# Performance work log

Measured on AMD Instinct MI355X. Metric: run time of the kernel, lower is better.

## Reference

```python
import jax, jax.numpy as jnp
import numpy as np

NUM_T = 1000      # diffusion timesteps
TIME_DIM = 16     # gaussian time embedding size
DIST_DIM = 16     # gaussian distance embedding size


def _gsmear(x, stop, num_g):
    # GaussianSmearing with linearly spaced centers in [0, stop]
    offsets = jnp.linspace(0.0, stop, num_g)
    coeff = -0.5 / (offsets[1] - offsets[0]) ** 2
    return jnp.exp(coeff * (x[:, None] - offsets[None, :]) ** 2)


def setup_inputs():
    key = jax.random.key(0)
    ks = jax.random.split(key, 20)
    N, EH, G = 20000, 100000, 1000          # nodes, halfedges, graphs
    NT, ND, ED, L, NE = 16, 256, 128, 2, 5   # node types, node_dim, edge_dim, blocks, edge types
    h_node = jax.nn.one_hot(jax.random.randint(ks[0], (N,), 0, NT), NT, dtype=jnp.float32)
    pos_node = jax.random.normal(ks[1], (N, 3), dtype=jnp.float32) * 3.0
    batch_node = jnp.sort(jax.random.randint(ks[2], (N,), 0, G))
    half = jax.random.randint(ks[3], (2, EH), 0, N)
    edge_index = jnp.concatenate([half, half[::-1]], axis=1)  # halfedges + flipped
    bh = jnp.sort(jax.random.randint(ks[4], (EH,), 0, G))
    batch_edge = jnp.concatenate([bh, bh], axis=0)
    t = jax.random.randint(ks[5], (G,), 0, NUM_T)

    def w(k, shape):
        fan_in = shape[-2] if len(shape) > 1 else shape[-1]
        return jax.random.normal(k, shape, dtype=jnp.float32) / np.sqrt(fan_in)

    e_in = ED + 2 * ND + DIST_DIM + 1
    return {
        'h_node': h_node, 'pos_node': pos_node, 'batch_node': batch_node,
        'edge_index': edge_index, 'batch_edge': batch_edge, 't': t,
        'W_node_emb': w(ks[6], (NT, ND - TIME_DIM)),
        'W_edge_emb': w(ks[7], (2 * NT, ED - TIME_DIM)),
        'We1': w(ks[8], (L, e_in, ED)), 'be1': jnp.zeros((L, ED), jnp.float32),
        'We2': w(ks[9], (L, ED, ED)), 'be2': jnp.zeros((L, ED), jnp.float32),
        'Wm': w(ks[10], (L, ND + ED, ND)), 'bm': jnp.zeros((L, ND), jnp.float32),
        'Wn1': w(ks[11], (L, 2 * ND + 1, ND)), 'bn1': jnp.zeros((L, ND), jnp.float32),
        'Wn2': w(ks[12], (L, ND, ND)), 'bn2': jnp.zeros((L, ND), jnp.float32),
        'Wd1': w(ks[13], (ED + ND, ED)), 'bd1': jnp.zeros((ED,), jnp.float32),
        'Wd2': w(ks[14], (ED, ED)), 'bd2': jnp.zeros((ED,), jnp.float32),
        'Wd3': w(ks[15], (ED, NE)), 'bd3': jnp.zeros((NE,), jnp.float32),
    }


def reference(h_node, pos_node, batch_node, edge_index, batch_edge, t,
              W_node_emb, W_edge_emb, We1, be1, We2, be2, Wm, bm,
              Wn1, bn1, Wn2, bn2, Wd1, bd1, Wd2, bd2, Wd3, bd3):
    src, dst = edge_index[0], edge_index[1]
    N = h_node.shape[0]
    L = We1.shape[0]

    # edge input features: concat of endpoint node features (gather)
    h_e0 = jnp.concatenate([h_node[src], h_node[dst]], axis=-1)

    tn = t[batch_node].astype(jnp.float32)  # per-node timestep
    te = t[batch_edge].astype(jnp.float32)  # per-edge timestep
    # linear embed + gaussian-smeared time embedding
    h_n = jnp.concatenate([h_node @ W_node_emb, _gsmear(tn, float(NUM_T), TIME_DIM)], axis=-1)
    h_e = jnp.concatenate([h_e0 @ W_edge_emb, _gsmear(te, float(NUM_T), TIME_DIM)], axis=-1)
    node_time = (tn / NUM_T)[:, None]
    edge_time = (te / NUM_T)[:, None]

    # geometric edge features
    d = jnp.linalg.norm(pos_node[dst] - pos_node[src], axis=-1)
    dist_emb = _gsmear(d, 10.0, DIST_DIM)

    # NodeEdgeNet: alternating edge / node residual updates
    for l in range(L):
        e_in = jnp.concatenate([h_e, h_n[src], h_n[dst], dist_emb, edge_time], axis=-1)
        h_e = h_e + jax.nn.relu(e_in @ We1[l] + be1[l]) @ We2[l] + be2[l]
        msg = jax.nn.relu(jnp.concatenate([h_n[src], h_e], axis=-1) @ Wm[l] + bm[l])
        agg = jax.ops.segment_sum(msg, dst, num_segments=N)
        n_in = jnp.concatenate([h_n, agg, node_time], axis=-1)
        h_n = h_n + jax.nn.relu(n_in @ Wn1[l] + bn1[l]) @ Wn2[l] + bn2[l]

    # symmetrize halfedges and decode edge types
    nh = h_e.shape[0] // 2
    h_ext = jnp.concatenate([h_e[:nh] + h_e[nh:],
                             h_n[src[:nh]] + h_n[dst[:nh]]], axis=-1)
    h = jax.nn.relu(h_ext @ Wd1 + bd1)
    h = jax.nn.relu(h @ Wd2 + bd2)
    return h @ Wd3 + bd3
```

## Files before the change

kernel.cpp:

```cpp
#include <hip/hip_runtime.h>
#include <math.h>


typedef __attribute__((ext_vector_type(8)))  short bf16x8;
typedef __attribute__((ext_vector_type(16))) float f32x16;

__device__ __forceinline__ float b2f(unsigned short u) {
    union { float f; unsigned int i; } x; x.i = ((unsigned int)u) << 16; return x.f;
}
__device__ __forceinline__ unsigned short f2b(float f) {
    union { float f; unsigned int i; } x; x.f = f;
    unsigned int r = x.i + 0x7fffu + ((x.i >> 16) & 1u);
    return (unsigned short)(r >> 16);
}
__device__ __forceinline__ bf16x8 ld8(const unsigned short* p) { return *(const bf16x8*)p; }
__device__ __forceinline__ bf16x8 zero8() { bf16x8 r = {0,0,0,0,0,0,0,0}; return r; }
__device__ __forceinline__ bf16x8 add8(bf16x8 a, bf16x8 b) {
    bf16x8 r;
#pragma unroll
    for (int j = 0; j < 8; j++) r[j] = (short)f2b(b2f((unsigned short)a[j]) + b2f((unsigned short)b[j]));
    return r;
}

#define MFMA4(ACC, A0, A1, B0, B1)                                                   \
    ACC[0][0] = __builtin_amdgcn_mfma_f32_32x32x16_bf16(A0, B0, ACC[0][0], 0, 0, 0); \
    ACC[0][1] = __builtin_amdgcn_mfma_f32_32x32x16_bf16(A0, B1, ACC[0][1], 0, 0, 0); \
    ACC[1][0] = __builtin_amdgcn_mfma_f32_32x32x16_bf16(A1, B0, ACC[1][0], 0, 0, 0); \
    ACC[1][1] = __builtin_amdgcn_mfma_f32_32x32x16_bf16(A1, B1, ACC[1][1], 0, 0, 0);

#define LANE_SETUP()                                  \
    const int tid  = threadIdx.x;                     \
    const int lane = tid & 63;                        \
    const int wave = tid >> 6;                        \
    const int wm = wave >> 1, wn = wave & 1;          \
    const int l31 = lane & 31, l5 = lane >> 5;        \
    (void)wm; (void)wn; (void)lane;

#define PIPELINE4(NITER, FETCH, ACC)                                  \
    {                                                                 \
        bf16x8 pa0[2], pb0[2], pa1[2], pb1[2], pa2[2], pb2[2];        \
        FETCH(0, pa0, pb0);                                           \
        if (1 < (NITER)) FETCH(1, pa1, pb1);                          \
        _Pragma("unroll")                                             \
        for (int i = 0; i < (NITER); i++) {                           \
            if (i + 2 < (NITER)) FETCH(i + 2, pa2, pb2);              \
            MFMA4(ACC, pa0[0], pa0[1], pb0[0], pb0[1]);               \
            pa0[0] = pa1[0]; pa0[1] = pa1[1];                         \
            pb0[0] = pb1[0]; pb0[1] = pb1[1];                         \
            pa1[0] = pa2[0]; pa1[1] = pa2[1];                         \
            pb1[0] = pb2[0]; pb1[1] = pb2[1];                         \
        }                                                             \
    }

__global__ void zero_i32_k(int* p, int n) {
    int i = blockIdx.x * 256 + threadIdx.x;
    if (i < n) p[i] = 0;
}
__global__ void hist_k(const int* __restrict__ dst, int* __restrict__ cnt, int E) {
    int e = blockIdx.x * 256 + threadIdx.x;
    if (e < E) atomicAdd(&cnt[dst[e]], 1);
}
__global__ __launch_bounds__(256) void scan_k(int* __restrict__ cnt, int N) {
    __shared__ int s[256];
    const int tidx  = threadIdx.x;
    const int chunk = (N + 255) / 256;
    const int lo = tidx * chunk;
    const int hi = (lo + chunk < N) ? lo + chunk : N;
    int sum = 0;
    for (int i = lo; i < hi; i++) sum += cnt[i];
    s[tidx] = sum;
    __syncthreads();
    for (int d = 1; d < 256; d <<= 1) {
        int t = (tidx >= d) ? s[tidx - d] : 0;
        __syncthreads();
        s[tidx] += t;
        __syncthreads();
    }
    int base = s[tidx] - sum;
    for (int i = lo; i < hi; i++) {
        int c = cnt[i];
        cnt[i] = base;
        base += c;
    }
}
__global__ void fill_k(const int* __restrict__ src, const int* __restrict__ dst,
                       const int* __restrict__ batch_edge, int* __restrict__ cur,
                       int* __restrict__ eids, int* __restrict__ pos,
                       int* __restrict__ srcp, int* __restrict__ dstp,
                       int* __restrict__ bep, int E) {
    int e = blockIdx.x * 256 + threadIdx.x;
    if (e < E) {
        int p = atomicAdd(&cur[dst[e]], 1);
        eids[p] = e;
        pos[e]  = p;
        srcp[p] = src[e];
        dstp[p] = dst[e];
        bep[p]  = batch_edge[e];
    }
}
__global__ void pad_k(int* eids, int* srcp, int* dstp, int* bep, int E, int Epad) {
    int i = E + blockIdx.x * 256 + threadIdx.x;
    if (i < Epad) { eids[i] = -1; srcp[i] = 0; dstp[i] = -1; bep[i] = 0; }
}

__global__ void typ_k(const float* __restrict__ h_node, int* __restrict__ typ, int N) {
    int i = blockIdx.x * 256 + threadIdx.x;
    if (i >= N) return;
    int ty = 0;
#pragma unroll
    for (int k = 0; k < 16; k++) if (h_node[i * 16 + k] > 0.5f) ty = k;
    typ[i] = ty;
}

struct TrDesc { const float* W; unsigned short* Wt; int K, N, Kpad; };
struct TrAll  { TrDesc d[12]; };

__global__ __launch_bounds__(256) void tr_all_k(TrAll a) {
    TrDesc t = a.d[blockIdx.y];
    int total = t.N * t.Kpad;
    for (int i = blockIdx.x * 256 + threadIdx.x; i < total; i += gridDim.x * 256) {
        int n = i / t.Kpad, k = i - n * t.Kpad;
        float v = (k < t.K) ? t.W[(size_t)k * t.N + n] : 0.f;
        t.Wt[(size_t)n * t.Kpad + k] = f2b(v);
    }
}

__global__ void embed_node_k(const int* __restrict__ typ,
                             const float* __restrict__ Wn,
                             const int* __restrict__ batch_node,
                             const int* __restrict__ t,
                             unsigned short* __restrict__ h_n, int N) {
    int idx = blockIdx.x * 256 + threadIdx.x;
    if (idx >= N * 32) return;
    int row = idx >> 5, seg = idx & 31;
    bf16x8 v;
    if (seg < 30) {
        const float* w = Wn + (size_t)typ[row] * 240 + seg * 8;
#pragma unroll
        for (int j = 0; j < 8; j++) v[j] = (short)f2b(w[j]);
    } else {
        float x = (float)t[batch_node[row]];
#pragma unroll
        for (int j = 0; j < 8; j++) {
            int col = seg * 8 + j;
            float dx = x - (1000.0f / 15.0f) * (float)(col - 240);
            v[j] = (short)f2b(expf(-1.125e-4f * dx * dx));
        }
    }
    *(bf16x8*)&h_n[(size_t)row * 256 + seg * 8] = v;
}

__global__ void embed_edge_k(const int* __restrict__ typ,
                             const float* __restrict__ We,
                             const int* __restrict__ srcp,
                             const int* __restrict__ dstp,
                             const int* __restrict__ bep,
                             const int* __restrict__ t,
                             unsigned short* __restrict__ h_e, int E) {
    int idx = blockIdx.x * 256 + threadIdx.x;
    if (idx >= E * 16) return;
    int row = idx >> 4, seg = idx & 15;
    bf16x8 v;
    if (seg < 14) {
        int d0 = dstp[row]; if (d0 < 0) d0 = 0;
        const float* ws = We + (size_t)typ[srcp[row]] * 112 + seg * 8;
        const float* wd = We + (size_t)(16 + typ[d0]) * 112 + seg * 8;
#pragma unroll
        for (int j = 0; j < 8; j++) v[j] = (short)f2b(ws[j] + wd[j]);
    } else {
        float x = (float)t[bep[row]];
#pragma unroll
        for (int j = 0; j < 8; j++) {
            int col = seg * 8 + j;
            float dx = x - (1000.0f / 15.0f) * (float)(col - 112);
            v[j] = (short)f2b(expf(-1.125e-4f * dx * dx));
        }
    }
    *(bf16x8*)&h_e[(size_t)row * 128 + seg * 8] = v;
}

__global__ __launch_bounds__(256) void edge_fused_k(
    unsigned short* __restrict__ h_e, const unsigned short* __restrict__ h_n,
    const unsigned short* __restrict__ Wt1, const float* __restrict__ be1,
    const unsigned short* __restrict__ Wt2, const float* __restrict__ be2,
    const float* __restrict__ pos, const int* __restrict__ srcp,
    const int* __restrict__ dstp, const int* __restrict__ t,
    const int* __restrict__ bep, int E)
{
    __shared__ __align__(16) char smem[128 * 136 * 2];
    unsigned short (*As)[8][8] = (unsigned short(*)[8][8])smem;
    unsigned short (*Bs)[8][8] = (unsigned short(*)[8][8])(smem + 16384);
    unsigned short (*H)[136]   = (unsigned short(*)[136])smem;

    LANE_SETUP();
    const int row0 = blockIdx.x * 128;
    const int srow = tid >> 3, sks = tid & 7;

    int rge[4], sg[4], dg[4]; bool okr[4];
#pragma unroll
    for (int p = 0; p < 4; p++) {
        int r = row0 + srow + p * 32;
        okr[p] = r < E;
        rge[p] = okr[p] ? r : 0;
        sg[p]  = srcp[rge[p]];
        dg[p]  = dstp[rge[p]]; if (dg[p] < 0) dg[p] = 0;
    }

    f32x16 acc[2][2] = {};
    for (int kc = 0; kc < 11; kc++) {
        const int cg = kc * 8 + sks;
#pragma unroll
        for (int p = 0; p < 4; p++) {
            int row = srow + p * 32;
            bf16x8 v;
            if (!okr[p] || cg >= 83) {
                v = zero8();
            } else if (cg < 16) {
                v = ld8(h_e + (size_t)rge[p] * 128 + (cg << 3));
            } else if (cg < 48) {
                v = ld8(h_n + (size_t)sg[p] * 256 + ((cg - 16) << 3));
            } else if (cg < 80) {
                v = ld8(h_n + (size_t)dg[p] * 256 + ((cg - 48) << 3));
            } else if (cg < 82) {
                float dx = pos[dg[p] * 3 + 0] - pos[sg[p] * 3 + 0];
                float dy = pos[dg[p] * 3 + 1] - pos[sg[p] * 3 + 1];
                float dz = pos[dg[p] * 3 + 2] - pos[sg[p] * 3 + 2];
                float dist = sqrtf(dx * dx + dy * dy + dz * dz);
#pragma unroll
                for (int j = 0; j < 8; j++) {
                    float u = dist - (10.0f / 15.0f) * (float)((cg - 80) * 8 + j);
                    v[j] = (short)f2b(expf(-1.125f * u * u));
                }
            } else {
                v = zero8();
                v[0] = (short)f2b((float)t[bep[rge[p]]] * 1e-3f);
            }
            *(bf16x8*)&As[row][sks ^ (row & 7)][0] = v;
        }
#pragma unroll
        for (int p = 0; p < 4; p++) {
            int col = srow + p * 32;
            bf16x8 v = (cg < 84) ? ld8(Wt1 + (size_t)col * 672 + (cg << 3)) : zero8();
            *(bf16x8*)&Bs[col][sks ^ (col & 7)][0] = v;
        }
        __syncthreads();
#pragma unroll
        for (int s = 0; s < 4; s++) {
            const int ks  = s * 2 + l5;
            const int ra0 = wm * 64 + l31, ra1 = ra0 + 32;
            const int ca0 = wn * 64 + l31, ca1 = ca0 + 32;
            bf16x8 a0 = *(const bf16x8*)&As[ra0][ks ^ (ra0 & 7)][0];
            bf16x8 a1 = *(const bf16x8*)&As[ra1][ks ^ (ra1 & 7)][0];
            bf16x8 b0 = *(const bf16x8*)&Bs[ca0][ks ^ (ca0 & 7)][0];
            bf16x8 b1 = *(const bf16x8*)&Bs[ca1][ks ^ (ca1 & 7)][0];
            MFMA4(acc, a0, a1, b0, b1);
        }
        __syncthreads();
    }

#pragma unroll
    for (int mt = 0; mt < 2; mt++)
#pragma unroll
        for (int nt = 0; nt < 2; nt++)
#pragma unroll
            for (int r = 0; r < 16; r++) {
                int lrow = wm * 64 + mt * 32 + (r & 3) + 8 * (r >> 2) + 4 * l5;
                int col  = wn * 64 + nt * 32 + l31;
                float v = acc[mt][nt][r] + be1[col];
                H[lrow][col] = f2b(fmaxf(v, 0.f));
            }
    __syncthreads();

    const unsigned short* W2a = Wt2 + (size_t)(wn * 64 + l31) * 128;
    const unsigned short* W2b = Wt2 + (size_t)(wn * 64 + 32 + l31) * 128;
    f32x16 acc2[2][2] = {};
#define EF2_FETCH(i, A, B)                                          \
    {                                                               \
        const int c = 2 * (i) + l5;                                 \
        A[0] = *(const bf16x8*)&H[wm * 64 + l31][c << 3];           \
        A[1] = *(const bf16x8*)&H[wm * 64 + 32 + l31][c << 3];      \
        B[0] = ld8(W2a + (c << 3));                                 \
        B[1] = ld8(W2b + (c << 3));                                 \
    }
    PIPELINE4(8, EF2_FETCH, acc2)
#undef EF2_FETCH

#pragma unroll
    for (int mt = 0; mt < 2; mt++)
#pragma unroll
        for (int nt = 0; nt < 2; nt++)
#pragma unroll
            for (int r = 0; r < 16; r++) {
                int lrow = wm * 64 + mt * 32 + (r & 3) + 8 * (r >> 2) + 4 * l5;
                int grow = row0 + lrow;
                if (grow >= E) continue;
                int col = wn * 64 + nt * 32 + l31;
                size_t off = (size_t)grow * 128 + col;
                float v = acc2[mt][nt][r] + be2[col] + b2f(h_e[off]);
                h_e[off] = f2b(v);
            }
}

__global__ __launch_bounds__(256) void msg_k(
    const unsigned short* __restrict__ h_e, const unsigned short* __restrict__ h_n,
    const unsigned short* __restrict__ Wtm, const float* __restrict__ bm,
    const int* __restrict__ srcp, const int* __restrict__ dstp,
    float* __restrict__ agg, int E)
{
    __shared__ __align__(16) char smem[49152 + 512];
    unsigned short (*As)[8][8]  = (unsigned short(*)[8][8])smem;
    unsigned short (*Bs0)[8][8] = (unsigned short(*)[8][8])(smem + 16384);
    unsigned short (*Bs1)[8][8] = (unsigned short(*)[8][8])(smem + 32768);
    float (*T)[129] = (float(*)[129])smem;
    int* dstv = (int*)(smem + 49152);

    LANE_SETUP();
    const int row0 = blockIdx.x * 128;

    if (tid < 128) dstv[tid] = dstp[row0 + tid];

    const int srow = tid >> 3, sks = tid & 7;

    f32x16 acc[2][2][2] = {};
    for (int kc = 0; kc < 6; kc++) {
        const int cg = kc * 8 + sks;
#pragma unroll
        for (int p = 0; p < 4; p++) {
            int row = srow + p * 32;
            int r   = row0 + row;
            bf16x8 v;
            if (r < E) {
                if (cg < 32) v = ld8(h_n + (size_t)srcp[r] * 256 + (cg << 3));
                else         v = ld8(h_e + (size_t)r * 128 + ((cg - 32) << 3));
            } else v = zero8();
            *(bf16x8*)&As[row][sks ^ (row & 7)][0] = v;
        }
#pragma unroll
        for (int p = 0; p < 4; p++) {
            int col = srow + p * 32;
            bf16x8 v0 = ld8(Wtm + (size_t)col * 384 + (cg << 3));
            bf16x8 v1 = ld8(Wtm + (size_t)(128 + col) * 384 + (cg << 3));
            *(bf16x8*)&Bs0[col][sks ^ (col & 7)][0] = v0;
            *(bf16x8*)&Bs1[col][sks ^ (col & 7)][0] = v1;
        }
        __syncthreads();
#pragma unroll
        for (int s = 0; s < 4; s++) {
            const int ks  = s * 2 + l5;
            const int ra0 = wm * 64 + l31, ra1 = ra0 + 32;
            const int ca0 = wn * 64 + l31, ca1 = ca0 + 32;
            bf16x8 a0  = *(const bf16x8*)&As[ra0][ks ^ (ra0 & 7)][0];
            bf16x8 a1  = *(const bf16x8*)&As[ra1][ks ^ (ra1 & 7)][0];
            bf16x8 b00 = *(const bf16x8*)&Bs0[ca0][ks ^ (ca0 & 7)][0];
            bf16x8 b01 = *(const bf16x8*)&Bs0[ca1][ks ^ (ca1 & 7)][0];
            bf16x8 b10 = *(const bf16x8*)&Bs1[ca0][ks ^ (ca0 & 7)][0];
            bf16x8 b11 = *(const bf16x8*)&Bs1[ca1][ks ^ (ca1 & 7)][0];
            MFMA4(acc[0], a0, a1, b00, b01);
            MFMA4(acc[1], a0, a1, b10, b11);
        }
        __syncthreads();
    }

    for (int ch = 0; ch < 2; ch++) {
        const int col0 = ch * 128;
        for (int ph = 0; ph < 2; ph++) {
            __syncthreads();
            if (wm == ph) {
#pragma unroll
                for (int mt = 0; mt < 2; mt++)
#pragma unroll
                    for (int nt = 0; nt < 2; nt++)
#pragma unroll
                        for (int r = 0; r < 16; r++) {
                            int lrow = mt * 32 + (r & 3) + 8 * (r >> 2) + 4 * l5;
                            int col  = wn * 64 + nt * 32 + l31;
                            T[lrow][col] = acc[ch][mt][nt][r] + bm[col0 + col];
                        }
            }
            __syncthreads();
            const int col = tid & 127, seg = tid >> 7;
            const int gcol = col0 + col;
            float run = 0.f; int prev = -1;
#pragma unroll 4
            for (int i = 0; i < 32; i++) {
                int lr = seg * 32 + i;
                int d  = dstv[ph * 64 + lr];
                float v = fmaxf(T[lr][col], 0.f);
                if (d != prev) {
                    if (prev >= 0 && run != 0.f) atomicAdd(&agg[(size_t)prev * 256 + gcol], run);
                    run = 0.f; prev = d;
                }
                if (d >= 0) run += v;
            }
            if (prev >= 0 && run != 0.f) atomicAdd(&agg[(size_t)prev * 256 + gcol], run);
        }
    }
}

__global__ __launch_bounds__(256) void nin_k(
    const unsigned short* __restrict__ h_n, const float* __restrict__ agg,
    const unsigned short* __restrict__ Wtn1, const float* __restrict__ bn1,
    const int* __restrict__ batch_node, const int* __restrict__ t,
    unsigned short* __restrict__ Hn, int N)
{
    __shared__ __align__(16) char smem[32768];
    unsigned short (*As)[8][8] = (unsigned short(*)[8][8])smem;
    unsigned short (*Bs)[8][8] = (unsigned short(*)[8][8])(smem + 16384);

    LANE_SETUP();
    const int row0 = blockIdx.x * 128;
    const int col0 = blockIdx.y * 128;
    const int srow = tid >> 3, sks = tid & 7;

    int rg[4]; bool okr[4]; float tv[4];
#pragma unroll
    for (int p = 0; p < 4; p++) {
        int r = row0 + srow + p * 32;
        okr[p] = r < N;
        rg[p]  = okr[p] ? r : 0;
        tv[p]  = (float)t[batch_node[rg[p]]] * 1e-3f;
    }

    f32x16 acc[2][2] = {};
    for (int kc = 0; kc < 9; kc++) {
        const int cg = kc * 8 + sks;
#pragma unroll
        for (int p = 0; p < 4; p++) {
            int row = srow + p * 32;
            bf16x8 v;
            if (!okr[p] || cg > 64) v = zero8();
            else if (cg < 32) v = ld8(h_n + (size_t)rg[p] * 256 + (cg << 3));
            else if (cg < 64) {
                const float* q = agg + (size_t)rg[p] * 256 + ((cg - 32) << 3);
#pragma unroll
                for (int j = 0; j < 8; j++) v[j] = (short)f2b(q[j]);
            } else { v = zero8(); v[0] = (short)f2b(tv[p]); }
            *(bf16x8*)&As[row][sks ^ (row & 7)][0] = v;
        }
#pragma unroll
        for (int p = 0; p < 4; p++) {
            int col = srow + p * 32;
            bf16x8 v = (cg < 68) ? ld8(Wtn1 + (size_t)(col0 + col) * 544 + (cg << 3)) : zero8();
            *(bf16x8*)&Bs[col][sks ^ (col & 7)][0] = v;
        }
        __syncthreads();
#pragma unroll
        for (int s = 0; s < 4; s++) {
            const int ks  = s * 2 + l5;
            const int ra0 = wm * 64 + l31, ra1 = ra0 + 32;
            const int ca0 = wn * 64 + l31, ca1 = ca0 + 32;
            bf16x8 a0 = *(const bf16x8*)&As[ra0][ks ^ (ra0 & 7)][0];
            bf16x8 a1 = *(const bf16x8*)&As[ra1][ks ^ (ra1 & 7)][0];
            bf16x8 b0 = *(const bf16x8*)&Bs[ca0][ks ^ (ca0 & 7)][0];
            bf16x8 b1 = *(const bf16x8*)&Bs[ca1][ks ^ (ca1 & 7)][0];
            MFMA4(acc, a0, a1, b0, b1);
        }
        __syncthreads();
    }

#pragma unroll
    for (int mt = 0; mt < 2; mt++)
#pragma unroll
        for (int nt = 0; nt < 2; nt++)
#pragma unroll
            for (int r = 0; r < 16; r++) {
                int lrow = wm * 64 + mt * 32 + (r & 3) + 8 * (r >> 2) + 4 * l5;
                int grow = row0 + lrow;
                if (grow >= N) continue;
                int col = col0 + wn * 64 + nt * 32 + l31;
                float v = fmaxf(acc[mt][nt][r] + bn1[col], 0.f);
                Hn[(size_t)grow * 256 + col] = f2b(v);
            }
}

__global__ __launch_bounds__(256) void node_plain_k(
    const unsigned short* __restrict__ Hn, const unsigned short* __restrict__ Wtn2,
    const float* __restrict__ bn2, unsigned short* __restrict__ h_n, int N)
{
    __shared__ __align__(16) char smem[32768];
    unsigned short (*As)[8][8] = (unsigned short(*)[8][8])smem;
    unsigned short (*Bs)[8][8] = (unsigned short(*)[8][8])(smem + 16384);

    LANE_SETUP();
    const int row0 = blockIdx.x * 128;
    const int col0 = blockIdx.y * 128;
    const int srow = tid >> 3, sks = tid & 7;

    f32x16 acc[2][2] = {};
    for (int kc = 0; kc < 4; kc++) {
        const int cg = kc * 8 + sks;
#pragma unroll
        for (int p = 0; p < 4; p++) {
            int row = srow + p * 32;
            int r   = row0 + row;
            bf16x8 v = (r < N) ? ld8(Hn + (size_t)r * 256 + (cg << 3)) : zero8();
            *(bf16x8*)&As[row][sks ^ (row & 7)][0] = v;
        }
#pragma unroll
        for (int p = 0; p < 4; p++) {
            int col = srow + p * 32;
            bf16x8 v = ld8(Wtn2 + (size_t)(col0 + col) * 256 + (cg << 3));
            *(bf16x8*)&Bs[col][sks ^ (col & 7)][0] = v;
        }
        __syncthreads();
#pragma unroll
        for (int s = 0; s < 4; s++) {
            const int ks  = s * 2 + l5;
            const int ra0 = wm * 64 + l31, ra1 = ra0 + 32;
            const int ca0 = wn * 64 + l31, ca1 = ca0 + 32;
            bf16x8 a0 = *(const bf16x8*)&As[ra0][ks ^ (ra0 & 7)][0];
            bf16x8 a1 = *(const bf16x8*)&As[ra1][ks ^ (ra1 & 7)][0];
            bf16x8 b0 = *(const bf16x8*)&Bs[ca0][ks ^ (ca0 & 7)][0];
            bf16x8 b1 = *(const bf16x8*)&Bs[ca1][ks ^ (ca1 & 7)][0];
            MFMA4(acc, a0, a1, b0, b1);
        }
        __syncthreads();
    }

#pragma unroll
    for (int mt = 0; mt < 2; mt++)
#pragma unroll
        for (int nt = 0; nt < 2; nt++)
#pragma unroll
            for (int r = 0; r < 16; r++) {
                int lrow = wm * 64 + mt * 32 + (r & 3) + 8 * (r >> 2) + 4 * l5;
                int grow = row0 + lrow;
                if (grow >= N) continue;
                int col = col0 + wn * 64 + nt * 32 + l31;
                size_t off = (size_t)grow * 256 + col;
                float v = acc[mt][nt][r] + bn2[col] + b2f(h_n[off]);
                h_n[off] = f2b(v);
            }
}

__global__ __launch_bounds__(256) void dec_fused_k(
    const unsigned short* __restrict__ h_e, const unsigned short* __restrict__ h_n,
    const unsigned short* __restrict__ Wtd1, const float* __restrict__ bd1,
    const unsigned short* __restrict__ Wtd2, const float* __restrict__ bd2,
    const float* __restrict__ Wd3, const float* __restrict__ bd3,
    const int* __restrict__ src, const int* __restrict__ dst,
    const int* __restrict__ pos, float* __restrict__ out, int nh)
{
    __shared__ __align__(16) char smem[128 * 136 * 2];
    __shared__ __align__(16) unsigned short H2[128][136];
    unsigned short (*As)[8][8] = (unsigned short(*)[8][8])smem;
    unsigned short (*Bs)[8][8] = (unsigned short(*)[8][8])(smem + 16384);
    unsigned short (*H1)[136]  = (unsigned short(*)[136])smem;

    LANE_SETUP();
    const int row0 = blockIdx.x * 128;
    const int srow = tid >> 3, sks = tid & 7;

    const unsigned short *pe1[4], *pe2[4], *pns[4], *pnd[4]; bool okr[4];
#pragma unroll
    for (int p = 0; p < 4; p++) {
        int r = row0 + srow + p * 32;
        okr[p] = r < nh;
        int rg = okr[p] ? r : 0;
        pe1[p] = h_e + (size_t)pos[rg] * 128;
        pe2[p] = h_e + (size_t)pos[rg + nh] * 128;
        pns[p] = h_n + (size_t)src[rg] * 256;
        pnd[p] = h_n + (size_t)dst[rg] * 256;
    }

    f32x16 acc[2][2] = {};
    for (int kc = 0; kc < 6; kc++) {
        const int cg = kc * 8 + sks;
#pragma unroll
        for (int p = 0; p < 4; p++) {
            int row = srow + p * 32;
            bf16x8 v;
            if (!okr[p]) v = zero8();
            else if (cg < 16) v = add8(ld8(pe1[p] + (cg << 3)), ld8(pe2[p] + (cg << 3)));
            else              v = add8(ld8(pns[p] + ((cg - 16) << 3)), ld8(pnd[p] + ((cg - 16) << 3)));
            *(bf16x8*)&As[row][sks ^ (row & 7)][0] = v;
        }
#pragma unroll
        for (int p = 0; p < 4; p++) {
            int col = srow + p * 32;
            bf16x8 v = ld8(Wtd1 + (size_t)col * 384 + (cg << 3));
            *(bf16x8*)&Bs[col][sks ^ (col & 7)][0] = v;
        }
        __syncthreads();
#pragma unroll
        for (int s = 0; s < 4; s++) {
            const int ks  = s * 2 + l5;
            const int ra0 = wm * 64 + l31, ra1 = ra0 + 32;
            const int ca0 = wn * 64 + l31, ca1 = ca0 + 32;
            bf16x8 a0 = *(const bf16x8*)&As[ra0][ks ^ (ra0 & 7)][0];
            bf16x8 a1 = *(const bf16x8*)&As[ra1][ks ^ (ra1 & 7)][0];
            bf16x8 b0 = *(const bf16x8*)&Bs[ca0][ks ^ (ca0 & 7)][0];
            bf16x8 b1 = *(const bf16x8*)&Bs[ca1][ks ^ (ca1 & 7)][0];
            MFMA4(acc, a0, a1, b0, b1);
        }
        __syncthreads();
    }

#pragma unroll
    for (int mt = 0; mt < 2; mt++)
#pragma unroll
        for (int nt = 0; nt < 2; nt++)
#pragma unroll
            for (int r = 0; r < 16; r++) {
                int lrow = wm * 64 + mt * 32 + (r & 3) + 8 * (r >> 2) + 4 * l5;
                int col  = wn * 64 + nt * 32 + l31;
                H1[lrow][col] = f2b(fmaxf(acc[mt][nt][r] + bd1[col], 0.f));
            }
    __syncthreads();

    const unsigned short* W2a = Wtd2 + (size_t)(wn * 64 + l31) * 128;
    const unsigned short* W2b = Wtd2 + (size_t)(wn * 64 + 32 + l31) * 128;
    f32x16 acc2[2][2] = {};
#define DC2_FETCH(i, A, B)                                          \
    {                                                               \
        const int c = 2 * (i) + l5;                                 \
        A[0] = *(const bf16x8*)&H1[wm * 64 + l31][c << 3];          \
        A[1] = *(const bf16x8*)&H1[wm * 64 + 32 + l31][c << 3];     \
        B[0] = ld8(W2a + (c << 3));                                 \
        B[1] = ld8(W2b + (c << 3));                                 \
    }
    PIPELINE4(8, DC2_FETCH, acc2)
#undef DC2_FETCH

#pragma unroll
    for (int mt = 0; mt < 2; mt++)
#pragma unroll
        for (int nt = 0; nt < 2; nt++)
#pragma unroll
            for (int r = 0; r < 16; r++) {
                int lrow = wm * 64 + mt * 32 + (r & 3) + 8 * (r >> 2) + 4 * l5;
                int col  = wn * 64 + nt * 32 + l31;
                H2[lrow][col] = f2b(fmaxf(acc2[mt][nt][r] + bd2[col], 0.f));
            }
    __syncthreads();

    if (tid < 128) {
        int grow = row0 + tid;
        if (grow < nh) {
            float a5[5] = {0.f, 0.f, 0.f, 0.f, 0.f};
            for (int ks = 0; ks < 16; ks++) {
                bf16x8 hv = *(const bf16x8*)&H2[tid][ks << 3];
#pragma unroll
                for (int j = 0; j < 8; j++) {
                    float a = b2f((unsigned short)hv[j]);
                    int   k = ks * 8 + j;
#pragma unroll
                    for (int c5 = 0; c5 < 5; c5++) a5[c5] += a * Wd3[k * 5 + c5];
                }
            }
#pragma unroll
            for (int c5 = 0; c5 < 5; c5++) out[(size_t)grow * 5 + c5] = a5[c5] + bd3[c5];
        }
    }
}


__global__ void zero_k(float* p, long n) {
    long i = (long)blockIdx.x * 256 + threadIdx.x;
    if (i < n) p[i] = 0.f;
}


extern "C" void kernel_launch(void* const* d_in, const int* in_sizes, int n_in,
                              void* d_out, int out_size, void* d_ws, size_t ws_size,
                              hipStream_t stream) {
    const float* h_node     = (const float*)d_in[0];
    const float* pos_node   = (const float*)d_in[1];
    const int*   batch_node = (const int*)d_in[2];
    const int*   edge_index = (const int*)d_in[3];
    const int*   batch_edge = (const int*)d_in[4];
    const int*   t          = (const int*)d_in[5];
    const float* W_node_emb = (const float*)d_in[6];
    const float* W_edge_emb = (const float*)d_in[7];
    const float* We1 = (const float*)d_in[8];
    const float* be1 = (const float*)d_in[9];
    const float* We2 = (const float*)d_in[10];
    const float* be2 = (const float*)d_in[11];
    const float* Wm  = (const float*)d_in[12];
    const float* bm  = (const float*)d_in[13];
    const float* Wn1 = (const float*)d_in[14];
    const float* bn1 = (const float*)d_in[15];
    const float* Wn2 = (const float*)d_in[16];
    const float* bn2 = (const float*)d_in[17];
    const float* Wd1 = (const float*)d_in[18];
    const float* bd1 = (const float*)d_in[19];
    const float* Wd2 = (const float*)d_in[20];
    const float* bd2 = (const float*)d_in[21];
    const float* Wd3 = (const float*)d_in[22];
    const float* bd3 = (const float*)d_in[23];

    const int N  = in_sizes[0] / 16;
    const int E  = in_sizes[3] / 2;
    const int nh = E / 2;
    const int* src = edge_index;
    const int* dst = edge_index + E;

    const int gE    = (E + 127) / 128;
    const int gN128 = (N + 127) / 128;
    const int Epad  = gE * 128;

    float* agg  = (float*)d_ws;
    int*   cnt  = (int*)(agg + (size_t)N * 256);
    int*   eids = cnt + N;
    int*   pos  = eids + Epad;
    int*   srcp = pos + Epad;
    int*   dstp = srcp + Epad;
    int*   bep  = dstp + Epad;
    int*   typ  = bep + Epad;
    unsigned short* h_e = (unsigned short*)(typ + N);
    unsigned short* h_n = h_e + (size_t)E * 128;
    unsigned short* Hn  = h_n + (size_t)N * 256;
    unsigned short* Wt1  = Hn + (size_t)N * 256;
    unsigned short* Wt2  = Wt1 + 2 * 128 * 672;
    unsigned short* Wtm  = Wt2 + 2 * 128 * 128;
    unsigned short* Wtn1 = Wtm + 2 * 256 * 384;
    unsigned short* Wtn2 = Wtn1 + 2 * 256 * 544;
    unsigned short* Wtd1 = Wtn2 + 2 * 256 * 256;
    unsigned short* Wtd2 = Wtd1 + 128 * 384;

    zero_i32_k<<<(N + 255) / 256, 256, 0, stream>>>(cnt, N);
    hist_k<<<(E + 255) / 256, 256, 0, stream>>>(dst, cnt, E);
    scan_k<<<1, 256, 0, stream>>>(cnt, N);
    fill_k<<<(E + 255) / 256, 256, 0, stream>>>(src, dst, batch_edge, cnt,
                                                eids, pos, srcp, dstp, bep, E);
    if (Epad > E) pad_k<<<1, 256, 0, stream>>>(eids, srcp, dstp, bep, E, Epad);
    typ_k<<<(N + 255) / 256, 256, 0, stream>>>(h_node, typ, N);

    TrAll ta;
    for (int l = 0; l < 2; l++) {
        ta.d[l * 5 + 0] = { We1 + (size_t)l * 657 * 128, Wt1 + (size_t)l * 128 * 672, 657, 128, 672 };
        ta.d[l * 5 + 1] = { We2 + (size_t)l * 128 * 128, Wt2 + (size_t)l * 128 * 128, 128, 128, 128 };
        ta.d[l * 5 + 2] = { Wm  + (size_t)l * 384 * 256, Wtm + (size_t)l * 256 * 384, 384, 256, 384 };
        ta.d[l * 5 + 3] = { Wn1 + (size_t)l * 513 * 256, Wtn1 + (size_t)l * 256 * 544, 513, 256, 544 };
        ta.d[l * 5 + 4] = { Wn2 + (size_t)l * 256 * 256, Wtn2 + (size_t)l * 256 * 256, 256, 256, 256 };
    }
    ta.d[10] = { Wd1, Wtd1, 384, 128, 384 };
    ta.d[11] = { Wd2, Wtd2, 128, 128, 128 };
    tr_all_k<<<dim3(48, 12), 256, 0, stream>>>(ta);

    embed_node_k<<<(N * 32 + 255) / 256, 256, 0, stream>>>(typ, W_node_emb, batch_node, t, h_n, N);
    embed_edge_k<<<(E * 16 + 255) / 256, 256, 0, stream>>>(typ, W_edge_emb, srcp, dstp, bep, t, h_e, E);

    for (int l = 0; l < 2; l++) {
        edge_fused_k<<<gE, 256, 0, stream>>>(
            h_e, h_n, Wt1 + (size_t)l * 128 * 672, be1 + l * 128,
            Wt2 + (size_t)l * 128 * 128, be2 + l * 128,
            pos_node, srcp, dstp, t, bep, E);

        zero_k<<<(int)(((long)N * 256 + 255) / 256), 256, 0, stream>>>(agg, (long)N * 256);
        msg_k<<<gE, 256, 0, stream>>>(
            h_e, h_n, Wtm + (size_t)l * 256 * 384, bm + l * 256, srcp, dstp, agg, E);

        nin_k<<<dim3(gN128, 2), 256, 0, stream>>>(
            h_n, agg, Wtn1 + (size_t)l * 256 * 544, bn1 + l * 256, batch_node, t, Hn, N);

        node_plain_k<<<dim3(gN128, 2), 256, 0, stream>>>(
            Hn, Wtn2 + (size_t)l * 256 * 256, bn2 + l * 256, h_n, N);
    }

    dec_fused_k<<<(nh + 127) / 128, 256, 0, stream>>>(
        h_e, h_n, Wtd1, bd1, Wtd2, bd2, Wd3, bd3, src, dst, pos, (float*)d_out, nh);
}
```

Before: 1.035 ms.

## Split message GEMM into two column-half blocks per row tile with grouped mapping

The message kernel now computes a 128x128 output tile per block instead of 128x256, doubling the grid and halving the accumulators and B-tile shared memory. Block indices are grouped so that two column halves of eight consecutive row tiles run close together, which should let the gathered A rows (h_n[src], h_e) hit in cache when read a second time. The aim is higher occupancy and lower register and LDS pressure, at the cost of gathering and staging the A operand twice.

```diff
diff --git a/kernel.cpp b/kernel.cpp
--- a/kernel.cpp
+++ b/kernel.cpp
@@ -305,23 +305,27 @@
     const unsigned short* __restrict__ h_e, const unsigned short* __restrict__ h_n,
     const unsigned short* __restrict__ Wtm, const float* __restrict__ bm,
     const int* __restrict__ srcp, const int* __restrict__ dstp,
-    float* __restrict__ agg, int E)
+    float* __restrict__ agg, int E, int nRowTiles)
 {
-    __shared__ __align__(16) char smem[49152 + 512];
-    unsigned short (*As)[8][8]  = (unsigned short(*)[8][8])smem;
-    unsigned short (*Bs0)[8][8] = (unsigned short(*)[8][8])(smem + 16384);
-    unsigned short (*Bs1)[8][8] = (unsigned short(*)[8][8])(smem + 32768);
+    __shared__ __align__(16) char smem[33024 + 512];
+    unsigned short (*As)[8][8] = (unsigned short(*)[8][8])smem;
+    unsigned short (*Bs)[8][8] = (unsigned short(*)[8][8])(smem + 16384);
     float (*T)[129] = (float(*)[129])smem;
-    int* dstv = (int*)(smem + 49152);
+    int* dstv = (int*)(smem + 33024);
 
     LANE_SETUP();
-    const int row0 = blockIdx.x * 128;
+    const int b    = blockIdx.x;
+    const int rowt = (b >> 4) * 8 + (b & 7);
+    const int colh = (b >> 3) & 1;
+    if (rowt >= nRowTiles) return;
+    const int row0 = rowt * 128;
+    const int col0 = colh * 128;
 
     if (tid < 128) dstv[tid] = dstp[row0 + tid];
 
     const int srow = tid >> 3, sks = tid & 7;
 
-    f32x16 acc[2][2][2] = {};
+    f32x16 acc[2][2] = {};
     for (int kc = 0; kc < 6; kc++) {
         const int cg = kc * 8 + sks;
 #pragma unroll
@@ -338,10 +342,8 @@
 #pragma unroll
         for (int p = 0; p < 4; p++) {
             int col = srow + p * 32;
-            bf16x8 v0 = ld8(Wtm + (size_t)col * 384 + (cg << 3));
-            bf16x8 v1 = ld8(Wtm + (size_t)(128 + col) * 384 + (cg << 3));
-            *(bf16x8*)&Bs0[col][sks ^ (col & 7)][0] = v0;
-            *(bf16x8*)&Bs1[col][sks ^ (col & 7)][0] = v1;
+            bf16x8 v = ld8(Wtm + (size_t)(col0 + col) * 384 + (cg << 3));
+            *(bf16x8*)&Bs[col][sks ^ (col & 7)][0] = v;
         }
         __syncthreads();
 #pragma unroll
@@ -349,51 +351,45 @@
             const int ks  = s * 2 + l5;
             const int ra0 = wm * 64 + l31, ra1 = ra0 + 32;
             const int ca0 = wn * 64 + l31, ca1 = ca0 + 32;
-            bf16x8 a0  = *(const bf16x8*)&As[ra0][ks ^ (ra0 & 7)][0];
-            bf16x8 a1  = *(const bf16x8*)&As[ra1][ks ^ (ra1 & 7)][0];
-            bf16x8 b00 = *(const bf16x8*)&Bs0[ca0][ks ^ (ca0 & 7)][0];
-            bf16x8 b01 = *(const bf16x8*)&Bs0[ca1][ks ^ (ca1 & 7)][0];
-            bf16x8 b10 = *(const bf16x8*)&Bs1[ca0][ks ^ (ca0 & 7)][0];
-            bf16x8 b11 = *(const bf16x8*)&Bs1[ca1][ks ^ (ca1 & 7)][0];
-            MFMA4(acc[0], a0, a1, b00, b01);
-            MFMA4(acc[1], a0, a1, b10, b11);
-        }
-        __syncthreads();
-    }
-
-    for (int ch = 0; ch < 2; ch++) {
-        const int col0 = ch * 128;
-        for (int ph = 0; ph < 2; ph++) {
-            __syncthreads();
-            if (wm == ph) {
-#pragma unroll
-                for (int mt = 0; mt < 2; mt++)
-#pragma unroll
-                    for (int nt = 0; nt < 2; nt++)
-#pragma unroll
-                        for (int r = 0; r < 16; r++) {
-                            int lrow = mt * 32 + (r & 3) + 8 * (r >> 2) + 4 * l5;
-                            int col  = wn * 64 + nt * 32 + l31;
-                            T[lrow][col] = acc[ch][mt][nt][r] + bm[col0 + col];
-                        }
-            }
-            __syncthreads();
-            const int col = tid & 127, seg = tid >> 7;
-            const int gcol = col0 + col;
-            float run = 0.f; int prev = -1;
+            bf16x8 a0 = *(const bf16x8*)&As[ra0][ks ^ (ra0 & 7)][0];
+            bf16x8 a1 = *(const bf16x8*)&As[ra1][ks ^ (ra1 & 7)][0];
+            bf16x8 b0 = *(const bf16x8*)&Bs[ca0][ks ^ (ca0 & 7)][0];
+            bf16x8 b1 = *(const bf16x8*)&Bs[ca1][ks ^ (ca1 & 7)][0];
+            MFMA4(acc, a0, a1, b0, b1);
+        }
+        __syncthreads();
+    }
+
+    for (int ph = 0; ph < 2; ph++) {
+        __syncthreads();
+        if (wm == ph) {
+#pragma unroll
+            for (int mt = 0; mt < 2; mt++)
+#pragma unroll
+                for (int nt = 0; nt < 2; nt++)
+#pragma unroll
+                    for (int r = 0; r < 16; r++) {
+                        int lrow = mt * 32 + (r & 3) + 8 * (r >> 2) + 4 * l5;
+                        int col  = wn * 64 + nt * 32 + l31;
+                        T[lrow][col] = acc[mt][nt][r] + bm[col0 + col];
+                    }
+        }
+        __syncthreads();
+        const int col = tid & 127, seg = tid >> 7;
+        const int gcol = col0 + col;
+        float run = 0.f; int prev = -1;
 #pragma unroll 4
-            for (int i = 0; i < 32; i++) {
-                int lr = seg * 32 + i;
-                int d  = dstv[ph * 64 + lr];
-                float v = fmaxf(T[lr][col], 0.f);
-                if (d != prev) {
-                    if (prev >= 0 && run != 0.f) atomicAdd(&agg[(size_t)prev * 256 + gcol], run);
-                    run = 0.f; prev = d;
-                }
-                if (d >= 0) run += v;
-            }
-            if (prev >= 0 && run != 0.f) atomicAdd(&agg[(size_t)prev * 256 + gcol], run);
-        }
+        for (int i = 0; i < 32; i++) {
+            int lr = seg * 32 + i;
+            int d  = dstv[ph * 64 + lr];
+            float v = fmaxf(T[lr][col], 0.f);
+            if (d != prev) {
+                if (prev >= 0 && run != 0.f) atomicAdd(&agg[(size_t)prev * 256 + gcol], run);
+                run = 0.f; prev = d;
+            }
+            if (d >= 0) run += v;
+        }
+        if (prev >= 0 && run != 0.f) atomicAdd(&agg[(size_t)prev * 256 + gcol], run);
     }
 }
 
@@ -696,6 +692,7 @@
     const int* dst = edge_index + E;
 
     const int gE    = (E + 127) / 128;
+    const int gE8   = ((gE + 7) / 8) * 8;
     const int gN128 = (N + 127) / 128;
     const int Epad  = gE * 128;
 
@@ -748,8 +745,8 @@
             pos_node, srcp, dstp, t, bep, E);
 
         zero_k<<<(int)(((long)N * 256 + 255) / 256), 256, 0, stream>>>(agg, (long)N * 256);
-        msg_k<<<gE, 256, 0, stream>>>(
-            h_e, h_n, Wtm + (size_t)l * 256 * 384, bm + l * 256, srcp, dstp, agg, E);
+        msg_k<<<gE8 * 2, 256, 0, stream>>>(
+            h_e, h_n, Wtm + (size_t)l * 256 * 384, bm + l * 256, srcp, dstp, agg, E, gE);
 
         nin_k<<<dim3(gN128, 2), 256, 0, stream>>>(
             h_n, agg, Wtn1 + (size_t)l * 256 * 544, bn1 + l * 256, batch_node, t, Hn, N);
```

After: 985.8 us. 4.7% less time.
